# Kernel tuning notes

Hardware: AMD Instinct MI355X
Metric: run time of the kernel (lower is better)

The kernel has to match this reference:

```python
import jax, jax.numpy as jnp
import numpy as np

EMBED_DIM = 768
NUM_HEADS = 12
HEAD_DIM = EMBED_DIM // NUM_HEADS


def setup_inputs() -> dict:
    key = jax.random.key(0)
    k1, k2, k3, k4, k5 = jax.random.split(key, 5)
    B, S, D = 2, 4096, EMBED_DIM
    scale = 1.0 / np.sqrt(D)
    return {
        "x": jax.random.normal(k1, (B, S, D), dtype=jnp.float32),
        "Wqkv": jax.random.normal(k2, (D, 3 * D), dtype=jnp.float32) * scale,
        "bqkv": jax.random.normal(k3, (3 * D,), dtype=jnp.float32) * 0.02,
        "Wout": jax.random.normal(k4, (D, D), dtype=jnp.float32) * scale,
        "bout": jax.random.normal(k5, (D,), dtype=jnp.float32) * 0.02,
    }


def reference(x, Wqkv, bqkv, Wout, bout):
    B, S, D = x.shape
    H, Hd = NUM_HEADS, HEAD_DIM
    # fused QKV projection: [B,S,3D]
    qkv = x @ Wqkv + bqkv
    q, k, v = jnp.split(qkv, 3, axis=-1)
    # [B,S,D] -> [B,H,S,Hd]
    q = q.reshape(B, S, H, Hd).transpose(0, 2, 1, 3)
    k = k.reshape(B, S, H, Hd).transpose(0, 2, 1, 3)
    v = v.reshape(B, S, H, Hd).transpose(0, 2, 1, 3)
    # causal SDPA (dropout_p = 0)
    scores = jnp.einsum("bhsd,bhtd->bhst", q, k) / jnp.sqrt(jnp.asarray(Hd, x.dtype))
    causal = jnp.tril(jnp.ones((S, S), dtype=bool))  # [S,S]
    scores = jnp.where(causal[None, None], scores, jnp.finfo(x.dtype).min)
    attn = jax.nn.softmax(scores, axis=-1)
    y = jnp.einsum("bhst,bhtd->bhsd", attn, v)  # [B,H,S,Hd]
    y = y.transpose(0, 2, 1, 3).reshape(B, S, D)
    return y @ Wout + bout
```

## Files before the change

### kernel.cpp

```cpp
#include <hip/hip_runtime.h>

#define S_LEN 4096
#define NH 12
#define HD 64
#define DMODEL 768
#define BATCH 2
#define MTOT (BATCH * S_LEN)

typedef __bf16 bf16x8 __attribute__((ext_vector_type(8)));
typedef __bf16 bf16x4 __attribute__((ext_vector_type(4)));
typedef float f32x4 __attribute__((ext_vector_type(4)));
typedef float f32x8 __attribute__((ext_vector_type(8)));

#define SM_SCALE_LOG2E 0.18033688f

__device__ __forceinline__ f32x4 f32x4_zero() {
  f32x4 z = {0.f, 0.f, 0.f, 0.f};
  return z;
}

__device__ __forceinline__ void async16(const __bf16* g, void* l) {
  __builtin_amdgcn_global_load_lds(
      (const __attribute__((address_space(1))) void*)g,
      (__attribute__((address_space(3))) void*)l, 16, 0, 0);
}

__global__ __launch_bounds__(256) void cvt_f32_bf16(const float* __restrict__ in,
                                                    __bf16* __restrict__ out, int n8) {
  int i = blockIdx.x * 256 + threadIdx.x;
  if (i >= n8) return;
  f32x8 a = ((const f32x8*)in)[i];
  bf16x8 o;
#pragma unroll
  for (int j = 0; j < 8; ++j) o[j] = (__bf16)a[j];
  ((bf16x8*)out)[i] = o;
}

__global__ __launch_bounds__(256) void transpose_cvt(const float* __restrict__ in,
                                                     __bf16* __restrict__ out, int N) {
  __shared__ __bf16 t[64][72];
  int kb = blockIdx.x * 64, nb = blockIdx.y * 64;
  int c = threadIdx.x & 63, r0 = threadIdx.x >> 6;
#pragma unroll
  for (int i = 0; i < 16; ++i) {
    int r = r0 * 16 + i;
    t[c][r] = (__bf16)in[(size_t)(kb + r) * N + nb + c];
  }
  __syncthreads();
#pragma unroll
  for (int i = 0; i < 16; ++i) {
    int r = r0 * 16 + i;
    out[(size_t)(nb + r) * DMODEL + kb + c] = t[r][c];
  }
}

__device__ __forceinline__ void gemm128_bt(const __bf16* __restrict__ A,
                                           const __bf16* __restrict__ Bt,
                                           int m0, int n0, int K,
                                           __bf16* Alds, __bf16* Blds,
                                           f32x4 acc[4][4]) {
  const int tid = threadIdx.x;
  const int l = tid & 63, w = tid >> 6;
  const int wr = w >> 1, wc = w & 1;
  const int g = l >> 4, ln = l & 15;

  const int rr = tid >> 3;
  const int sx = (tid & 7) ^ (rr & 7);
  const __bf16* As = A + (size_t)(m0 + rr) * K + sx * 8;
  const __bf16* Bs = Bt + (size_t)(n0 + rr) * K + sx * 8;
  char* Ad = (char*)Alds + (w << 10);
  char* Bd = (char*)Blds + (w << 10);

  for (int k0 = 0; k0 < K; k0 += 64) {
#pragma unroll
    for (int i = 0; i < 4; ++i) {
      async16(As + (size_t)(i * 32) * K + k0, Ad + i * 4096);
      async16(Bs + (size_t)(i * 32) * K + k0, Bd + i * 4096);
    }
    __syncthreads();
#pragma unroll
    for (int kk = 0; kk < 2; ++kk) {
      bf16x8 af[4], bfr[4];
#pragma unroll
      for (int mi = 0; mi < 4; ++mi) {
        int row = wr * 64 + mi * 16 + ln;
        af[mi] = *(const bf16x8*)(Alds + row * 64 + ((((kk << 2) + g) ^ (row & 7)) << 3));
      }
#pragma unroll
      for (int ni = 0; ni < 4; ++ni) {
        int row = wc * 64 + ni * 16 + ln;
        bfr[ni] = *(const bf16x8*)(Blds + row * 64 + ((((kk << 2) + g) ^ (row & 7)) << 3));
      }
#pragma unroll
      for (int mi = 0; mi < 4; ++mi)
#pragma unroll
        for (int ni = 0; ni < 4; ++ni)
          acc[mi][ni] =
              __builtin_amdgcn_mfma_f32_16x16x32_bf16(af[mi], bfr[ni], acc[mi][ni], 0, 0, 0);
    }
    __syncthreads();
  }
}

__global__ __launch_bounds__(256) void gemm_qkv(const __bf16* __restrict__ xb,
                                                const __bf16* __restrict__ Wt,
                                                const float* __restrict__ bqkv,
                                                __bf16* __restrict__ Qo,
                                                __bf16* __restrict__ Ko,
                                                __bf16* __restrict__ Vto) {
  __shared__ __bf16 Alds[128 * 64];
  __shared__ __bf16 Blds[128 * 64];
  int bm = blockIdx.x & 63, bn = blockIdx.x >> 6;
  int m0 = bm * 128, n0 = bn * 128;
  f32x4 acc[4][4];
#pragma unroll
  for (int i = 0; i < 4; ++i)
#pragma unroll
    for (int j = 0; j < 4; ++j) acc[i][j] = f32x4_zero();
  gemm128_bt(xb, Wt, m0, n0, DMODEL, Alds, Blds, acc);

  const int l = threadIdx.x & 63, w = threadIdx.x >> 6;
  const int wr = w >> 1, wc = w & 1, g = l >> 4, ln = l & 15;
#pragma unroll
  for (int ni = 0; ni < 4; ++ni) {
    int ncol = n0 + wc * 64 + ni * 16 + ln;
    int which = ncol / DMODEL;
    int dd = ncol - which * DMODEL;
    int h = dd >> 6, hd = dd & 63;
    float bias = bqkv[ncol];
    if (which == 2) {
#pragma unroll
      for (int mi = 0; mi < 4; ++mi)
#pragma unroll
        for (int r = 0; r < 4; ++r) {
          int mrow = m0 + wr * 64 + mi * 16 + 4 * g + r;
          int b = mrow >> 12, s = mrow & (S_LEN - 1);
          float v = acc[mi][ni][r] + bias;
          Vto[(((size_t)(b * NH + h) * HD) + hd) * S_LEN + s] = (__bf16)v;
        }
    } else {
      __bf16* op = (which == 0) ? Qo : Ko;
      const float scl = (which == 0) ? SM_SCALE_LOG2E : 1.0f;
#pragma unroll
      for (int mi = 0; mi < 4; ++mi)
#pragma unroll
        for (int r = 0; r < 4; ++r) {
          int mrow = m0 + wr * 64 + mi * 16 + 4 * g + r;
          int b = mrow >> 12, s = mrow & (S_LEN - 1);
          float v = (acc[mi][ni][r] + bias) * scl;
          op[((((size_t)b * NH + h) * S_LEN) + s) * HD + hd] = (__bf16)v;
        }
    }
  }
}

__global__ __launch_bounds__(256) void gemm_out(const __bf16* __restrict__ yb,
                                                const __bf16* __restrict__ Wt,
                                                const float* __restrict__ bout,
                                                float* __restrict__ out) {
  __shared__ __bf16 Alds[128 * 64];
  __shared__ __bf16 Blds[128 * 64];
  int bm = blockIdx.x & 63, bn = blockIdx.x >> 6;
  int m0 = bm * 128, n0 = bn * 128;
  f32x4 acc[4][4];
#pragma unroll
  for (int i = 0; i < 4; ++i)
#pragma unroll
    for (int j = 0; j < 4; ++j) acc[i][j] = f32x4_zero();
  gemm128_bt(yb, Wt, m0, n0, DMODEL, Alds, Blds, acc);

  const int l = threadIdx.x & 63, w = threadIdx.x >> 6;
  const int wr = w >> 1, wc = w & 1, g = l >> 4, ln = l & 15;
#pragma unroll
  for (int ni = 0; ni < 4; ++ni) {
    int ncol = n0 + wc * 64 + ni * 16 + ln;
    float bias = bout[ncol];
#pragma unroll
    for (int mi = 0; mi < 4; ++mi)
#pragma unroll
      for (int r = 0; r < 4; ++r) {
        int mrow = m0 + wr * 64 + mi * 16 + 4 * g + r;
        out[(size_t)mrow * DMODEL + ncol] = acc[mi][ni][r] + bias;
      }
  }
}

__global__ __launch_bounds__(256) void attn_fwd13(const __bf16* __restrict__ Q,
                                                  const __bf16* __restrict__ K,
                                                  const __bf16* __restrict__ Vt,
                                                  __bf16* __restrict__ Y) {
  __shared__ __bf16 KVl[2][2][4096];
  __shared__ char Plb[4][2048];

  const int tid = threadIdx.x;
  const int wv = tid >> 6, l = tid & 63;
  const int g = l >> 4, ln = l & 15;
  const int bi = blockIdx.x;
  const int xcd = bi & 7, j = bi >> 3;
  const int head = xcd * 3 + (j % 3);
  const int p = j / 3;
  const int hc = 63 - p;
  const int thr = 16 * wv + ln;

  const size_t hb = (size_t)head * (S_LEN * HD);
  const __bf16* Qh = Q + hb;
  const __bf16* Kh = K + hb;
  const __bf16* Vh = Vt + hb;

  const int q0H = 64 * hc + 16 * wv;
  const int q0L = 64 * p + 16 * wv;

  const int sw = (ln & 7) << 4;
  char* Pw = Plb[wv] + ln * 128;

  const int r0 = tid >> 3;
  const int s0 = (tid & 7) ^ (r0 & 7);
  const size_t kL0 = (size_t)r0 * HD + s0 * 8;
  const size_t kL1 = kL0 + (size_t)32 * HD;
  const size_t vL0 = (size_t)r0 * S_LEN + s0 * 8;
  const size_t vL1 = vL0 + (size_t)32 * S_LEN;
  const int ldsoff = wv << 10;

  bf16x8 qfH[2], qfL[2];
#pragma unroll
  for (int t = 0; t < 2; ++t) {
    qfH[t] = *(const bf16x8*)(Qh + (size_t)(q0H + ln) * HD + 32 * t + 8 * g);
    qfL[t] = *(const bf16x8*)(Qh + (size_t)(q0L + ln) * HD + 32 * t + 8 * g);
  }

  bf16x8 ones;
#pragma unroll
  for (int t = 0; t < 8; ++t) ones[t] = (__bf16)1.0f;

  f32x4 o[4], o5;
#pragma unroll
  for (int nt = 0; nt < 4; ++nt) o[nt] = f32x4_zero();
  o5 = f32x4_zero();

  const int bb = head / NH, hh = head - bb * NH;
  __bf16* Yp = Y + ((size_t)bb * S_LEN) * DMODEL + hh * HD;

  {
    char* Kd = (char*)&KVl[0][0][0] + ldsoff;
    char* Vd = (char*)&KVl[0][1][0] + ldsoff;
    async16(Kh + kL0, Kd);
    async16(Kh + kL1, Kd + 4096);
    async16(Vh + vL0, Vd);
    async16(Vh + vL1, Vd + 4096);
    __syncthreads();
  }
  const __bf16* kq = Kh + 64 * HD;
  const __bf16* vq = Vh + 64;

  int cur = 0;
  for (int i = 0; i < 65; ++i) {
    const bool more = i < 64;
    if (more) {
      if (i == hc) {
        kq = Kh;
        vq = Vh;
      }
      char* Kd = (char*)&KVl[cur ^ 1][0][0] + ldsoff;
      char* Vd = (char*)&KVl[cur ^ 1][1][0] + ldsoff;
      async16(kq + kL0, Kd);
      async16(kq + kL1, Kd + 4096);
      async16(vq + vL0, Vd);
      async16(vq + vL1, Vd + 4096);
      kq += (size_t)64 * HD;
      vq += 64;
    }

    const __bf16* Kl = &KVl[cur][0][0];
    const __bf16* Vl = &KVl[cur][1][0];
    const bool phL = (i > hc);
    const bool diag = (i == hc) || (i == 64);
    bf16x8 qf0 = phL ? qfL[0] : qfH[0];
    bf16x8 qf1 = phL ? qfL[1] : qfH[1];

    if (!diag) {
#pragma unroll
      for (int jt = 0; jt < 4; ++jt) {
        int row = 16 * jt + ln;
        bf16x8 kf0 = *(const bf16x8*)(Kl + row * 64 + ((g ^ (row & 7)) << 3));
        bf16x8 kf1 = *(const bf16x8*)(Kl + row * 64 + (((4 + g) ^ (row & 7)) << 3));
        f32x4 z = f32x4_zero();
        z = __builtin_amdgcn_mfma_f32_16x16x32_bf16(kf0, qf0, z, 0, 0, 0);
        z = __builtin_amdgcn_mfma_f32_16x16x32_bf16(kf1, qf1, z, 0, 0, 0);
        bf16x4 qd;
#pragma unroll
        for (int r = 0; r < 4; ++r) qd[r] = (__bf16)__builtin_exp2f(z[r]);
        *(bf16x4*)(Pw + ((32 * jt + 8 * g) ^ sw)) = qd;
      }
    } else {
#pragma unroll
      for (int jt = 0; jt < 4; ++jt) {
        int row = 16 * jt + ln;
        bf16x8 kf0 = *(const bf16x8*)(Kl + row * 64 + ((g ^ (row & 7)) << 3));
        bf16x8 kf1 = *(const bf16x8*)(Kl + row * 64 + (((4 + g) ^ (row & 7)) << 3));
        f32x4 z = f32x4_zero();
        z = __builtin_amdgcn_mfma_f32_16x16x32_bf16(kf0, qf0, z, 0, 0, 0);
        z = __builtin_amdgcn_mfma_f32_16x16x32_bf16(kf1, qf1, z, 0, 0, 0);
        bf16x4 qd;
#pragma unroll
        for (int r = 0; r < 4; ++r) {
          float pv = __builtin_exp2f(z[r]);
          if (16 * jt + 4 * g + r > thr) pv = 0.f;
          qd[r] = (__bf16)pv;
        }
        *(bf16x4*)(Pw + ((32 * jt + 8 * g) ^ sw)) = qd;
      }
    }

    bf16x8 pa0 = *(const bf16x8*)(Pw + ((16 * g) ^ sw));
    bf16x8 pa1 = *(const bf16x8*)(Pw + ((64 + 16 * g) ^ sw));
    __builtin_amdgcn_s_setprio(1);
    o5 = __builtin_amdgcn_mfma_f32_16x16x32_bf16(pa0, ones, o5, 0, 0, 0);
    o5 = __builtin_amdgcn_mfma_f32_16x16x32_bf16(pa1, ones, o5, 0, 0, 0);
#pragma unroll
    for (int nt = 0; nt < 4; ++nt) {
      int row = 16 * nt + ln;
      bf16x8 vf0 = *(const bf16x8*)(Vl + row * 64 + ((g ^ (row & 7)) << 3));
      bf16x8 vf1 = *(const bf16x8*)(Vl + row * 64 + (((4 + g) ^ (row & 7)) << 3));
      o[nt] = __builtin_amdgcn_mfma_f32_16x16x32_bf16(pa0, vf0, o[nt], 0, 0, 0);
      o[nt] = __builtin_amdgcn_mfma_f32_16x16x32_bf16(pa1, vf1, o[nt], 0, 0, 0);
    }
    __builtin_amdgcn_s_setprio(0);

    if (diag) {
      const int q0 = phL ? q0L : q0H;
#pragma unroll
      for (int r = 0; r < 4; ++r) {
        float inv = 1.0f / o5[r];
        int qr = q0 + 4 * g + r;
#pragma unroll
        for (int nt = 0; nt < 4; ++nt)
          Yp[(size_t)qr * DMODEL + 16 * nt + ln] = (__bf16)(o[nt][r] * inv);
      }
#pragma unroll
      for (int nt = 0; nt < 4; ++nt) o[nt] = f32x4_zero();
      o5 = f32x4_zero();
    }

    if (more) __syncthreads();
    cur ^= 1;
  }
}

extern "C" void kernel_launch(void* const* d_in, const int* in_sizes, int n_in,
                              void* d_out, int out_size, void* d_ws, size_t ws_size,
                              hipStream_t stream) {
  const float* x = (const float*)d_in[0];
  const float* Wqkv = (const float*)d_in[1];
  const float* bqkv = (const float*)d_in[2];
  const float* Wout = (const float*)d_in[3];
  const float* bout = (const float*)d_in[4];
  float* out = (float*)d_out;

  char* ws = (char*)d_ws;
  size_t off = 0;
  auto take = [&](size_t bytes) {
    char* p = ws + off;
    off += bytes;
    return p;
  };
  const size_t MD2 = (size_t)MTOT * DMODEL * 2;
  __bf16* xb = (__bf16*)take(MD2);
  __bf16* Wqkv_t = (__bf16*)take((size_t)3 * DMODEL * DMODEL * 2);
  __bf16* Wout_t = (__bf16*)take((size_t)DMODEL * DMODEL * 2);
  __bf16* Qb = (__bf16*)take(MD2);
  __bf16* Kb = (__bf16*)take(MD2);
  __bf16* Vtb = (__bf16*)take(MD2);
  __bf16* Yb = (__bf16*)take(MD2);

  int n8 = MTOT * DMODEL / 8;
  cvt_f32_bf16<<<(n8 + 255) / 256, 256, 0, stream>>>(x, xb, n8);
  transpose_cvt<<<dim3(DMODEL / 64, 3 * DMODEL / 64), 256, 0, stream>>>(Wqkv, Wqkv_t, 3 * DMODEL);
  transpose_cvt<<<dim3(DMODEL / 64, DMODEL / 64), 256, 0, stream>>>(Wout, Wout_t, DMODEL);
  gemm_qkv<<<64 * (3 * DMODEL / 128), 256, 0, stream>>>(xb, Wqkv_t, bqkv, Qb, Kb, Vtb);
  attn_fwd13<<<768, 256, 0, stream>>>(Qb, Kb, Vtb, Yb);
  gemm_out<<<64 * (DMODEL / 128), 256, 0, stream>>>(Yb, Wout_t, bout, out);
}
```

Baseline: 186.1 us.

## Split long causal attention rows across two blocks and combine partial sums

Replaces the paired high/low query-tile scheduling in attention with a split-KV scheme. The 32 longest query tiles per head are split into two halves processed by separate blocks, and the 32 shortest tiles run whole, giving 2304 blocks instead of 768. Split blocks write unnormalized bf16 partial outputs and row sums to a workspace, and a new combine kernel adds the halves and normalizes. This aims to balance work and raise parallelism, at the cost of an extra launch, extra global traffic and bf16 rounding of the partials. It relies on the softmax being computed without a running max, as before.

```diff
diff --git a/kernel.cpp b/kernel.cpp
--- a/kernel.cpp
+++ b/kernel.cpp
@@ -13,6 +13,7 @@
 typedef float f32x8 __attribute__((ext_vector_type(8)));
 
 #define SM_SCALE_LOG2E 0.18033688f
+#define SLAB_STRIDE 8448
 
 __device__ __forceinline__ f32x4 f32x4_zero() {
   f32x4 z = {0.f, 0.f, 0.f, 0.f};
@@ -185,10 +186,11 @@
   }
 }
 
-__global__ __launch_bounds__(256) void attn_fwd13(const __bf16* __restrict__ Q,
+__global__ __launch_bounds__(256) void attn_fwd14(const __bf16* __restrict__ Q,
                                                   const __bf16* __restrict__ K,
                                                   const __bf16* __restrict__ Vt,
-                                                  __bf16* __restrict__ Y) {
+                                                  __bf16* __restrict__ Y,
+                                                  char* __restrict__ Po) {
   __shared__ __bf16 KVl[2][2][4096];
   __shared__ char Plb[4][2048];
 
@@ -198,17 +200,33 @@
   const int bi = blockIdx.x;
   const int xcd = bi & 7, j = bi >> 3;
   const int head = xcd * 3 + (j % 3);
-  const int p = j / 3;
-  const int hc = 63 - p;
+  const int r_ = j / 3;
+
+  int c, t0, t1, part;
+  bool split;
+  if (r_ < 64) {
+    c = 63 - (r_ >> 1);
+    part = r_ & 1;
+    int T = c + 1;
+    int h = (T + 1) >> 1;
+    t0 = part ? h : 0;
+    t1 = part ? T : h;
+    split = true;
+  } else {
+    c = 95 - r_;
+    part = 0;
+    t0 = 0;
+    t1 = c + 1;
+    split = false;
+  }
+  const int q0 = 64 * c + 16 * wv;
   const int thr = 16 * wv + ln;
+  const bool hasDiag = (t1 == c + 1);
 
   const size_t hb = (size_t)head * (S_LEN * HD);
   const __bf16* Qh = Q + hb;
   const __bf16* Kh = K + hb;
   const __bf16* Vh = Vt + hb;
-
-  const int q0H = 64 * hc + 16 * wv;
-  const int q0L = 64 * p + 16 * wv;
 
   const int sw = (ln & 7) << 4;
   char* Pw = Plb[wv] + ln * 128;
@@ -221,12 +239,10 @@
   const size_t vL1 = vL0 + (size_t)32 * S_LEN;
   const int ldsoff = wv << 10;
 
-  bf16x8 qfH[2], qfL[2];
-#pragma unroll
-  for (int t = 0; t < 2; ++t) {
-    qfH[t] = *(const bf16x8*)(Qh + (size_t)(q0H + ln) * HD + 32 * t + 8 * g);
-    qfL[t] = *(const bf16x8*)(Qh + (size_t)(q0L + ln) * HD + 32 * t + 8 * g);
-  }
+  bf16x8 qf[2];
+#pragma unroll
+  for (int t = 0; t < 2; ++t)
+    qf[t] = *(const bf16x8*)(Qh + (size_t)(q0 + ln) * HD + 32 * t + 8 * g);
 
   bf16x8 ones;
 #pragma unroll
@@ -237,29 +253,24 @@
   for (int nt = 0; nt < 4; ++nt) o[nt] = f32x4_zero();
   o5 = f32x4_zero();
 
-  const int bb = head / NH, hh = head - bb * NH;
-  __bf16* Yp = Y + ((size_t)bb * S_LEN) * DMODEL + hh * HD;
-
+  const __bf16* kq = Kh + (size_t)t0 * 64 * HD;
+  const __bf16* vq = Vh + t0 * 64;
   {
     char* Kd = (char*)&KVl[0][0][0] + ldsoff;
     char* Vd = (char*)&KVl[0][1][0] + ldsoff;
-    async16(Kh + kL0, Kd);
-    async16(Kh + kL1, Kd + 4096);
-    async16(Vh + vL0, Vd);
-    async16(Vh + vL1, Vd + 4096);
+    async16(kq + kL0, Kd);
+    async16(kq + kL1, Kd + 4096);
+    async16(vq + vL0, Vd);
+    async16(vq + vL1, Vd + 4096);
     __syncthreads();
   }
-  const __bf16* kq = Kh + 64 * HD;
-  const __bf16* vq = Vh + 64;
+  kq += (size_t)64 * HD;
+  vq += 64;
 
   int cur = 0;
-  for (int i = 0; i < 65; ++i) {
-    const bool more = i < 64;
+  for (int i = t0; i < t1; ++i) {
+    const bool more = (i + 1) < t1;
     if (more) {
-      if (i == hc) {
-        kq = Kh;
-        vq = Vh;
-      }
       char* Kd = (char*)&KVl[cur ^ 1][0][0] + ldsoff;
       char* Vd = (char*)&KVl[cur ^ 1][1][0] + ldsoff;
       async16(kq + kL0, Kd);
@@ -272,10 +283,7 @@
 
     const __bf16* Kl = &KVl[cur][0][0];
     const __bf16* Vl = &KVl[cur][1][0];
-    const bool phL = (i > hc);
-    const bool diag = (i == hc) || (i == 64);
-    bf16x8 qf0 = phL ? qfL[0] : qfH[0];
-    bf16x8 qf1 = phL ? qfL[1] : qfH[1];
+    const bool diag = hasDiag && (i == c);
 
     if (!diag) {
 #pragma unroll
@@ -284,8 +292,8 @@
         bf16x8 kf0 = *(const bf16x8*)(Kl + row * 64 + ((g ^ (row & 7)) << 3));
         bf16x8 kf1 = *(const bf16x8*)(Kl + row * 64 + (((4 + g) ^ (row & 7)) << 3));
         f32x4 z = f32x4_zero();
-        z = __builtin_amdgcn_mfma_f32_16x16x32_bf16(kf0, qf0, z, 0, 0, 0);
-        z = __builtin_amdgcn_mfma_f32_16x16x32_bf16(kf1, qf1, z, 0, 0, 0);
+        z = __builtin_amdgcn_mfma_f32_16x16x32_bf16(kf0, qf[0], z, 0, 0, 0);
+        z = __builtin_amdgcn_mfma_f32_16x16x32_bf16(kf1, qf[1], z, 0, 0, 0);
         bf16x4 qd;
 #pragma unroll
         for (int r = 0; r < 4; ++r) qd[r] = (__bf16)__builtin_exp2f(z[r]);
@@ -298,8 +306,8 @@
         bf16x8 kf0 = *(const bf16x8*)(Kl + row * 64 + ((g ^ (row & 7)) << 3));
         bf16x8 kf1 = *(const bf16x8*)(Kl + row * 64 + (((4 + g) ^ (row & 7)) << 3));
         f32x4 z = f32x4_zero();
-        z = __builtin_amdgcn_mfma_f32_16x16x32_bf16(kf0, qf0, z, 0, 0, 0);
-        z = __builtin_amdgcn_mfma_f32_16x16x32_bf16(kf1, qf1, z, 0, 0, 0);
+        z = __builtin_amdgcn_mfma_f32_16x16x32_bf16(kf0, qf[0], z, 0, 0, 0);
+        z = __builtin_amdgcn_mfma_f32_16x16x32_bf16(kf1, qf[1], z, 0, 0, 0);
         bf16x4 qd;
 #pragma unroll
         for (int r = 0; r < 4; ++r) {
@@ -326,24 +334,56 @@
     }
     __builtin_amdgcn_s_setprio(0);
 
-    if (diag) {
-      const int q0 = phL ? q0L : q0H;
-#pragma unroll
-      for (int r = 0; r < 4; ++r) {
-        float inv = 1.0f / o5[r];
-        int qr = q0 + 4 * g + r;
-#pragma unroll
-        for (int nt = 0; nt < 4; ++nt)
-          Yp[(size_t)qr * DMODEL + 16 * nt + ln] = (__bf16)(o[nt][r] * inv);
-      }
-#pragma unroll
-      for (int nt = 0; nt < 4; ++nt) o[nt] = f32x4_zero();
-      o5 = f32x4_zero();
-    }
-
     if (more) __syncthreads();
     cur ^= 1;
   }
+
+  if (!split) {
+    const int bb = head / NH, hh = head - bb * NH;
+    __bf16* Yp = Y + ((size_t)bb * S_LEN) * DMODEL + hh * HD;
+#pragma unroll
+    for (int r = 0; r < 4; ++r) {
+      float inv = 1.0f / o5[r];
+      int qr = q0 + 4 * g + r;
+#pragma unroll
+      for (int nt = 0; nt < 4; ++nt)
+        Yp[(size_t)qr * DMODEL + 16 * nt + ln] = (__bf16)(o[nt][r] * inv);
+    }
+  } else {
+    char* slab = Po + (size_t)(((head << 5) + (c - 32)) * 2 + part) * SLAB_STRIDE;
+#pragma unroll
+    for (int r = 0; r < 4; ++r) {
+      int rowL = 16 * wv + 4 * g + r;
+#pragma unroll
+      for (int nt = 0; nt < 4; ++nt)
+        *(__bf16*)(slab + (rowL * 64 + 16 * nt + ln) * 2) = (__bf16)o[nt][r];
+      if (ln == 0) *(float*)(slab + 8192 + rowL * 4) = o5[r];
+    }
+  }
+}
+
+__global__ __launch_bounds__(256) void attn_combine(const char* __restrict__ Po,
+                                                    __bf16* __restrict__ Y) {
+  const int blk = blockIdx.x;
+  const int head = blk >> 6, rem = blk & 63;
+  const int cc = rem >> 1, half = rem & 1;
+  const int c = cc + 32;
+  const char* s0 = Po + (size_t)(((head << 5) + cc) * 2) * SLAB_STRIDE;
+  const char* s1 = s0 + SLAB_STRIDE;
+  const int tid = threadIdx.x;
+  const int row = half * 32 + (tid >> 3), d0 = (tid & 7) * 8;
+
+  bf16x8 a = *(const bf16x8*)(s0 + (row * 64 + d0) * 2);
+  bf16x8 b = *(const bf16x8*)(s1 + (row * 64 + d0) * 2);
+  float rs = *(const float*)(s0 + 8192 + row * 4) + *(const float*)(s1 + 8192 + row * 4);
+  float inv = 1.0f / rs;
+
+  const int bb = head / NH, hh = head - bb * NH;
+  __bf16* yp = Y + ((size_t)bb * S_LEN + 64 * c + row) * DMODEL + hh * HD + d0;
+  bf16x8 o;
+#pragma unroll
+  for (int j = 0; j < 8; ++j) o[j] = (__bf16)(((float)a[j] + (float)b[j]) * inv);
+  *(bf16x8*)yp = o;
 }
 
 extern "C" void kernel_launch(void* const* d_in, const int* in_sizes, int n_in,
@@ -371,12 +411,14 @@
   __bf16* Kb = (__bf16*)take(MD2);
   __bf16* Vtb = (__bf16*)take(MD2);
   __bf16* Yb = (__bf16*)take(MD2);
+  char* Po = take((size_t)1536 * SLAB_STRIDE);
 
   int n8 = MTOT * DMODEL / 8;
   cvt_f32_bf16<<<(n8 + 255) / 256, 256, 0, stream>>>(x, xb, n8);
   transpose_cvt<<<dim3(DMODEL / 64, 3 * DMODEL / 64), 256, 0, stream>>>(Wqkv, Wqkv_t, 3 * DMODEL);
   transpose_cvt<<<dim3(DMODEL / 64, DMODEL / 64), 256, 0, stream>>>(Wout, Wout_t, DMODEL);
   gemm_qkv<<<64 * (3 * DMODEL / 128), 256, 0, stream>>>(xb, Wqkv_t, bqkv, Qb, Kb, Vtb);
-  attn_fwd13<<<768, 256, 0, stream>>>(Qb, Kb, Vtb, Yb);
+  attn_fwd14<<<2304, 256, 0, stream>>>(Qb, Kb, Vtb, Yb, Po);
+  attn_combine<<<1536, 256, 0, stream>>>(Po, Yb);
   gemm_out<<<64 * (DMODEL / 128), 256, 0, stream>>>(Yb, Wout_t, bout, out);
 }
```

Result: no change. 183.2 us (-1.6%).
